# Optimization experiments

Measured on AMD Instinct MI355X. Metric: run time of the kernel, lower is better.

Reference implementation:

```python
import jax, jax.numpy as jnp
import numpy as np

NUM_HEADS = 8

def setup_inputs() -> dict:
    key0 = jax.random.key(0)
    ks = jax.random.split(key0, 6)
    T, S, B, E = 2048, 2048, 2, 256
    W_SCALE = 0.06  # ~xavier_uniform std for 256x256
    return {
        "query": jax.random.normal(ks[0], (T, B, E), dtype=jnp.float32),
        "key": jax.random.normal(ks[1], (S, B, E), dtype=jnp.float32),
        "value": jax.random.normal(ks[2], (S, B, E), dtype=jnp.float32),
        "Wq": jax.random.normal(ks[3], (E, E), dtype=jnp.float32) * W_SCALE,
        "bq": jnp.zeros((E,), dtype=jnp.float32),
        "Wk": jax.random.normal(ks[4], (E, E), dtype=jnp.float32) * W_SCALE,
        "bk": jnp.zeros((E,), dtype=jnp.float32),
        "Wo": jax.random.normal(ks[5], (E, E), dtype=jnp.float32) * W_SCALE,
        "bo": jnp.zeros((E,), dtype=jnp.float32),
    }

def reference(query, key, value, Wq, bq, Wk, bk, Wo, bo):
    # query: [T,B,E], key/value: [S,B,E]
    T, B, E = query.shape
    S = key.shape[0]
    H = NUM_HEADS
    Dh = E // H
    q = jnp.einsum('tbe,fe->tbf', query, Wq) + bq
    k = jnp.einsum('sbe,fe->sbf', key, Wk) + bk
    # split heads: view(L, B*H, Dh) == reshape(L, B, H, Dh)
    qh = q.reshape(T, B, H, Dh)
    kh = k.reshape(S, B, H, Dh)
    vh = value.reshape(S, B, H, Dh)  # v is NOT projected in this module
    scale = 1.0 / jnp.sqrt(jnp.asarray(Dh, dtype=query.dtype))
    scores = jnp.einsum('tbhd,sbhd->bhts', qh * scale, kh)  # [B,H,T,S]
    attn = jax.nn.softmax(scores, axis=-1)
    out = jnp.einsum('bhts,sbhd->tbhd', attn, vh).reshape(T, B, E)
    # residual output projection: out + linear(out)
    out = out + jnp.einsum('tbe,fe->tbf', out, Wo) + bo
    avg_weights = jnp.mean(attn, axis=1)  # [B,T,S]
    return (out, avg_weights)
```

## Files before the change

### kernel.cpp

```cpp
#include <hip/hip_runtime.h>
#include <hip/hip_fp16.h>

#define T_DIM 2048
#define S_DIM 2048
#define B_DIM 2
#define E_DIM 256
#define H_DIM 8
#define DH 32

typedef _Float16 half8 __attribute__((ext_vector_type(8)));
typedef _Float16 half4 __attribute__((ext_vector_type(4)));
typedef float floatx4 __attribute__((ext_vector_type(4)));

#if defined(__has_builtin)
#if __has_builtin(__builtin_amdgcn_exp2f)
#define EXPFN(x) __builtin_amdgcn_exp2f(x)
#define LOG2E_FOLD 1.4426950408889634f
#endif
#endif
#ifndef EXPFN
#define EXPFN(x) __expf(x)
#define LOG2E_FOLD 1.0f
#endif

__global__ __launch_bounds__(256) void prep_kernel(const float* __restrict__ V,
                                                   _Float16* __restrict__ Vt2,
                                                   const float* __restrict__ Wq,
                                                   const float* __restrict__ Wk,
                                                   const float* __restrict__ Wo,
                                                   _Float16* __restrict__ Wqh,
                                                   _Float16* __restrict__ Wkh,
                                                   _Float16* __restrict__ Woh) {
  __shared__ float tile[64][33];
  int tid = threadIdx.x;
  int bx = blockIdx.x;
  if (bx < 512) {
    int st = bx & 31, h = (bx >> 5) & 7, b = bx >> 8;
    int s0 = st * 64;
    int d = tid & 31, sr = tid >> 5;
#pragma unroll
    for (int k = 0; k < 8; ++k) {
      int s = sr + k * 8;
      tile[s][d] = V[((size_t)(s0 + s) * B_DIM + b) * E_DIM + h * DH + d];
    }
    __syncthreads();
    int si = tid & 63, dq = tid >> 6;
    size_t base = ((size_t)b * H_DIM + h) * 128 * 512;
    int tl = st * 4 + (si >> 4);
    int sl = si & 15;
#pragma unroll
    for (int m = 0; m < 8; ++m) {
      int dd = dq * 8 + m;
      Vt2[base + (size_t)tl * 512 + dd * 16 + sl] = (_Float16)tile[si][dd];
    }
  } else {
    int i = (bx - 512) * 2048 + tid * 8;
    int sel = i >> 16, off = i & 65535;
    const float* src = sel == 0 ? Wq : (sel == 1 ? Wk : Wo);
    _Float16* dst = sel == 0 ? Wqh : (sel == 1 ? Wkh : Woh);
    float4 a0 = *(const float4*)(src + off);
    float4 a1 = *(const float4*)(src + off + 4);
    half8 hv;
    hv[0]=(_Float16)a0.x; hv[1]=(_Float16)a0.y; hv[2]=(_Float16)a0.z; hv[3]=(_Float16)a0.w;
    hv[4]=(_Float16)a1.x; hv[5]=(_Float16)a1.y; hv[6]=(_Float16)a1.z; hv[7]=(_Float16)a1.w;
    if (sel == 2) {
      int f = off >> 8, e0 = off & 255;
      int di = f - e0;
      if (di >= 0 && di < 8) hv[di] += (_Float16)1.0f;
    }
    *(half8*)(dst + off) = hv;
  }
}

#define XS 264
__global__ __launch_bounds__(256, 4) void proj_mfma(const float* __restrict__ Q,
                                                    const float* __restrict__ K,
                                                    const _Float16* __restrict__ Wqh,
                                                    const _Float16* __restrict__ Wkh,
                                                    const float* __restrict__ bq,
                                                    const float* __restrict__ bk,
                                                    _Float16* __restrict__ Qp,
                                                    _Float16* __restrict__ Kp,
                                                    float scale_q) {
  __shared__ _Float16 Xs[64 * XS];
  int z = blockIdx.z;
  const float* X = z ? K : Q;
  const _Float16* Wh = z ? Wkh : Wqh;
  const float* bias = z ? bk : bq;
  _Float16* out = z ? Kp : Qp;
  float scale = z ? 1.0f : scale_q;

  int tid = threadIdx.x;
  int lane = tid & 63, w = tid >> 6;
  int quad = lane >> 4, l16 = lane & 15;
  int r0 = blockIdx.x * 64;
  int c0 = blockIdx.y * 64;

#pragma unroll
  for (int it = 0; it < 16; ++it) {
    int row = (tid >> 6) + it * 4, col = (tid & 63) * 4;
    float4 a = *(const float4*)(X + (size_t)(r0 + row) * 256 + col);
    half4 hv;
    hv[0] = (_Float16)a.x; hv[1] = (_Float16)a.y;
    hv[2] = (_Float16)a.z; hv[3] = (_Float16)a.w;
    *(half4*)(Xs + row * XS + col) = hv;
  }
  __syncthreads();

  floatx4 c[4] = {{0.f,0.f,0.f,0.f},{0.f,0.f,0.f,0.f},{0.f,0.f,0.f,0.f},{0.f,0.f,0.f,0.f}};
  int arow = w * 16 + l16;
#pragma unroll
  for (int k0 = 0; k0 < 256; k0 += 32) {
    half8 af = *(const half8*)(Xs + arow * XS + k0 + quad * 8);
#pragma unroll
    for (int j = 0; j < 4; ++j) {
      int f = c0 + j * 16 + l16;
      half8 bf = *(const half8*)(Wh + (size_t)f * 256 + k0 + quad * 8);
      c[j] = __builtin_amdgcn_mfma_f32_16x16x32_f16(af, bf, c[j], 0, 0, 0);
    }
  }
#pragma unroll
  for (int j = 0; j < 4; ++j) {
    int f = c0 + j * 16 + l16;
    float bv = bias[f];
    int h = f >> 5, d = f & 31;
#pragma unroll
    for (int r = 0; r < 4; ++r) {
      int row = r0 + w * 16 + quad * 4 + r;
      int t = row >> 1, b = row & 1;
      out[(((size_t)b * H_DIM + h) * T_DIM + t) * DH + d] =
          (_Float16)((c[j][r] + bv) * scale);
    }
  }
}

#define OSTRIDE 36
__global__ __launch_bounds__(1024, 4) void attn_fused(const _Float16* __restrict__ Qp,
                                                      const _Float16* __restrict__ Kp,
                                                      const _Float16* __restrict__ Vt2,
                                                      _Float16* __restrict__ Of16,
                                                      float* __restrict__ avg_out) {
  __shared__ float stageO[2][16][16 * OSTRIDE];
  __shared__ float lstage[2][16][16];

  int tid = threadIdx.x;
  int lane = tid & 63, w = tid >> 6;
  int quad = lane >> 4, l16 = lane & 15;
  int bx = blockIdx.x;
  int b = bx & 1, tc = bx >> 1;
  int t0 = tc << 4;
  int sbase = w << 7;
  int tl0 = w << 3;

  half4 avg_acc[8];
#pragma unroll
  for (int st = 0; st < 8; ++st) avg_acc[st] = (half4){0, 0, 0, 0};

  for (int h = 0; h < H_DIM; ++h) {
    const _Float16* Qb = Qp + (((size_t)b * H_DIM + h) * T_DIM + t0) * DH;
    const _Float16* Kb = Kp + ((size_t)b * H_DIM + h) * S_DIM * DH;
    const _Float16* Vb = Vt2 + ((size_t)b * H_DIM + h) * 128 * 512;

    half8 qfrag = *(const half8*)(Qb + (size_t)l16 * DH + quad * 8);
    floatx4 o0 = {0.f,0.f,0.f,0.f}, o1 = {0.f,0.f,0.f,0.f};
    float lacc = 0.f;
    half4 pst[8];

    half8 kf[2];
    half4 v0[2], v1[2];
    kf[0] = *(const half8*)(Kb + (size_t)(sbase + l16) * DH + quad * 8);
    v0[0] = *(const half4*)(Vb + (size_t)tl0 * 512 + l16 * 16 + quad * 4);
    v1[0] = *(const half4*)(Vb + (size_t)tl0 * 512 + 256 + l16 * 16 + quad * 4);

#pragma unroll
    for (int st = 0; st < 8; ++st) {
      int cur = st & 1, nxt = cur ^ 1;
      if (st < 7) {
        int tl = tl0 + st + 1;
        kf[nxt] = *(const half8*)(Kb + (size_t)(tl * 16 + l16) * DH + quad * 8);
        v0[nxt] = *(const half4*)(Vb + (size_t)tl * 512 + l16 * 16 + quad * 4);
        v1[nxt] = *(const half4*)(Vb + (size_t)tl * 512 + 256 + l16 * 16 + quad * 4);
      }
      floatx4 c = {0.f, 0.f, 0.f, 0.f};
      c = __builtin_amdgcn_mfma_f32_16x16x32_f16(kf[cur], qfrag, c, 0, 0, 0);
      float e0 = EXPFN(c[0]), e1 = EXPFN(c[1]), e2 = EXPFN(c[2]), e3 = EXPFN(c[3]);
      lacc += (e0 + e1) + (e2 + e3);
      half4 p;
      p[0] = (_Float16)e0; p[1] = (_Float16)e1; p[2] = (_Float16)e2; p[3] = (_Float16)e3;
      pst[st] = p;
      o0 = __builtin_amdgcn_mfma_f32_16x16x16f16(p, v0[cur], o0, 0, 0, 0);
      o1 = __builtin_amdgcn_mfma_f32_16x16x16f16(p, v1[cur], o1, 0, 0, 0);
    }

    int bufi = h & 1;
    lacc += __shfl_xor(lacc, 16, 64);
    lacc += __shfl_xor(lacc, 32, 64);
    if (quad == 0) lstage[bufi][w][l16] = lacc;
#pragma unroll
    for (int r = 0; r < 4; ++r) {
      stageO[bufi][w][(quad * 4 + r) * OSTRIDE + l16] = o0[r];
      stageO[bufi][w][(quad * 4 + r) * OSTRIDE + 16 + l16] = o1[r];
    }
    __syncthreads();

    float lrow = 0.f;
#pragma unroll
    for (int ww = 0; ww < 16; ++ww) lrow += lstage[bufi][ww][l16];
    _Float16 rlh = (_Float16)(1.0f / lrow);
    half4 rv; rv[0] = rlh; rv[1] = rlh; rv[2] = rlh; rv[3] = rlh;
#pragma unroll
    for (int st = 0; st < 8; ++st) avg_acc[st] += pst[st] * rv;

    if (tid < 512) {
      int t = tid >> 5, d = tid & 31;
      float osum = 0.f, lr = 0.f;
#pragma unroll
      for (int ww = 0; ww < 16; ++ww) {
        osum += stageO[bufi][ww][t * OSTRIDE + d];
        lr += lstage[bufi][ww][t];
      }
      Of16[((size_t)(t0 + t) * B_DIM + b) * E_DIM + h * DH + d] =
          (_Float16)(osum / lr);
    }
  }

  float* ao = avg_out + ((size_t)b * T_DIM + t0 + l16) * S_DIM + sbase + quad * 4;
#pragma unroll
  for (int st = 0; st < 8; ++st) {
    float4 o;
    o.x = (float)avg_acc[st][0] * 0.125f;
    o.y = (float)avg_acc[st][1] * 0.125f;
    o.z = (float)avg_acc[st][2] * 0.125f;
    o.w = (float)avg_acc[st][3] * 0.125f;
    *(float4*)(ao + st * 16) = o;
  }
}

__global__ __launch_bounds__(256, 4) void outproj_mfma(const _Float16* __restrict__ Of16,
                                                       const _Float16* __restrict__ Woh,
                                                       const float* __restrict__ bo,
                                                       float* __restrict__ out) {
  __shared__ _Float16 Os[64 * XS];
  int tid = threadIdx.x;
  int lane = tid & 63, w = tid >> 6;
  int quad = lane >> 4, l16 = lane & 15;
  int r0 = blockIdx.x * 64;
  int c0 = blockIdx.y * 64;

#pragma unroll
  for (int it = 0; it < 8; ++it) {
    int row = (tid >> 5) + it * 8, col = (tid & 31) * 8;
    *(half8*)(Os + row * XS + col) =
        *(const half8*)(Of16 + (size_t)(r0 + row) * 256 + col);
  }
  __syncthreads();

  floatx4 c[4] = {{0.f,0.f,0.f,0.f},{0.f,0.f,0.f,0.f},{0.f,0.f,0.f,0.f},{0.f,0.f,0.f,0.f}};
  int arow = w * 16 + l16;
#pragma unroll
  for (int k0 = 0; k0 < 256; k0 += 32) {
    half8 af = *(const half8*)(Os + arow * XS + k0 + quad * 8);
#pragma unroll
    for (int j = 0; j < 4; ++j) {
      int f = c0 + j * 16 + l16;
      half8 bf = *(const half8*)(Woh + (size_t)f * 256 + k0 + quad * 8);
      c[j] = __builtin_amdgcn_mfma_f32_16x16x32_f16(af, bf, c[j], 0, 0, 0);
    }
  }
#pragma unroll
  for (int j = 0; j < 4; ++j) {
    int f = c0 + j * 16 + l16;
    float bv = bo[f];
#pragma unroll
    for (int r = 0; r < 4; ++r) {
      int row = r0 + w * 16 + quad * 4 + r;
      out[(size_t)row * 256 + f] = c[j][r] + bv;
    }
  }
}

extern "C" void kernel_launch(void* const* d_in, const int* in_sizes, int n_in,
                              void* d_out, int out_size, void* d_ws, size_t ws_size,
                              hipStream_t stream) {
  const float* query = (const float*)d_in[0];
  const float* key   = (const float*)d_in[1];
  const float* value = (const float*)d_in[2];
  const float* Wq    = (const float*)d_in[3];
  const float* bq    = (const float*)d_in[4];
  const float* Wk    = (const float*)d_in[5];
  const float* bk    = (const float*)d_in[6];
  const float* Wo    = (const float*)d_in[7];
  const float* bo    = (const float*)d_in[8];

  float* out = (float*)d_out;
  float* avg_out = out + (size_t)T_DIM * B_DIM * E_DIM;

  char* ws = (char*)d_ws;
  _Float16* Qp   = (_Float16*)ws;
  _Float16* Kp   = (_Float16*)(ws + (2u << 20));
  _Float16* Vt2  = (_Float16*)(ws + (4u << 20));
  _Float16* Of16 = (_Float16*)(ws + (6u << 20));
  _Float16* Wqh  = (_Float16*)(ws + (8u << 20) + (128u << 10));
  _Float16* Wkh  = (_Float16*)(ws + (8u << 20) + (256u << 10));
  _Float16* Woh  = (_Float16*)(ws + (8u << 20) + (384u << 10));

  const float scale_q = 0.17677669529663687f * LOG2E_FOLD;

  prep_kernel<<<dim3(608), dim3(256), 0, stream>>>(value, Vt2, Wq, Wk, Wo, Wqh, Wkh, Woh);
  proj_mfma<<<dim3(64, 4, 2), dim3(256), 0, stream>>>(query, key, Wqh, Wkh, bq, bk,
                                                      Qp, Kp, scale_q);
  attn_fused<<<dim3(256), dim3(1024), 0, stream>>>(Qp, Kp, Vt2, Of16, avg_out);
  outproj_mfma<<<dim3(64, 4), dim3(256), 0, stream>>>(Of16, Woh, bo, out);
}
```

Before: 146.7 us.

## Fuse prep with QK projection and fold output projection into attention kernel

Measured after the change: 149.4 us. No clear change (+1.8%).

```diff
diff --git a/kernel.cpp b/kernel.cpp
--- a/kernel.cpp
+++ b/kernel.cpp
@@ -23,18 +23,24 @@
 #define LOG2E_FOLD 1.0f
 #endif
 
-__global__ __launch_bounds__(256) void prep_kernel(const float* __restrict__ V,
-                                                   _Float16* __restrict__ Vt2,
-                                                   const float* __restrict__ Wq,
-                                                   const float* __restrict__ Wk,
-                                                   const float* __restrict__ Wo,
-                                                   _Float16* __restrict__ Wqh,
-                                                   _Float16* __restrict__ Wkh,
-                                                   _Float16* __restrict__ Woh) {
-  __shared__ float tile[64][33];
+#define XS 264
+__global__ __launch_bounds__(256, 4) void prep_proj(const float* __restrict__ V,
+                                                    _Float16* __restrict__ Vt2,
+                                                    const float* __restrict__ Wo,
+                                                    _Float16* __restrict__ Woh,
+                                                    const float* __restrict__ Q,
+                                                    const float* __restrict__ K,
+                                                    const float* __restrict__ Wq,
+                                                    const float* __restrict__ Wk,
+                                                    const float* __restrict__ bq,
+                                                    const float* __restrict__ bk,
+                                                    _Float16* __restrict__ Qp,
+                                                    _Float16* __restrict__ Kp,
+                                                    float scale_q) {
   int tid = threadIdx.x;
   int bx = blockIdx.x;
   if (bx < 512) {
+    __shared__ float tile[64][33];
     int st = bx & 31, h = (bx >> 5) & 7, b = bx >> 8;
     int s0 = st * 64;
     int d = tid & 31, sr = tid >> 5;
@@ -53,83 +59,75 @@
       int dd = dq * 8 + m;
       Vt2[base + (size_t)tl * 512 + dd * 16 + sl] = (_Float16)tile[si][dd];
     }
-  } else {
+  } else if (bx < 544) {
     int i = (bx - 512) * 2048 + tid * 8;
-    int sel = i >> 16, off = i & 65535;
-    const float* src = sel == 0 ? Wq : (sel == 1 ? Wk : Wo);
-    _Float16* dst = sel == 0 ? Wqh : (sel == 1 ? Wkh : Woh);
-    float4 a0 = *(const float4*)(src + off);
-    float4 a1 = *(const float4*)(src + off + 4);
+    float4 a0 = *(const float4*)(Wo + i);
+    float4 a1 = *(const float4*)(Wo + i + 4);
     half8 hv;
     hv[0]=(_Float16)a0.x; hv[1]=(_Float16)a0.y; hv[2]=(_Float16)a0.z; hv[3]=(_Float16)a0.w;
     hv[4]=(_Float16)a1.x; hv[5]=(_Float16)a1.y; hv[6]=(_Float16)a1.z; hv[7]=(_Float16)a1.w;
-    if (sel == 2) {
-      int f = off >> 8, e0 = off & 255;
-      int di = f - e0;
-      if (di >= 0 && di < 8) hv[di] += (_Float16)1.0f;
-    }
-    *(half8*)(dst + off) = hv;
-  }
-}
-
-#define XS 264
-__global__ __launch_bounds__(256, 4) void proj_mfma(const float* __restrict__ Q,
-                                                    const float* __restrict__ K,
-                                                    const _Float16* __restrict__ Wqh,
-                                                    const _Float16* __restrict__ Wkh,
-                                                    const float* __restrict__ bq,
-                                                    const float* __restrict__ bk,
-                                                    _Float16* __restrict__ Qp,
-                                                    _Float16* __restrict__ Kp,
-                                                    float scale_q) {
-  __shared__ _Float16 Xs[64 * XS];
-  int z = blockIdx.z;
-  const float* X = z ? K : Q;
-  const _Float16* Wh = z ? Wkh : Wqh;
-  const float* bias = z ? bk : bq;
-  _Float16* out = z ? Kp : Qp;
-  float scale = z ? 1.0f : scale_q;
-
-  int tid = threadIdx.x;
-  int lane = tid & 63, w = tid >> 6;
-  int quad = lane >> 4, l16 = lane & 15;
-  int r0 = blockIdx.x * 64;
-  int c0 = blockIdx.y * 64;
-
-#pragma unroll
-  for (int it = 0; it < 16; ++it) {
-    int row = (tid >> 6) + it * 4, col = (tid & 63) * 4;
-    float4 a = *(const float4*)(X + (size_t)(r0 + row) * 256 + col);
-    half4 hv;
-    hv[0] = (_Float16)a.x; hv[1] = (_Float16)a.y;
-    hv[2] = (_Float16)a.z; hv[3] = (_Float16)a.w;
-    *(half4*)(Xs + row * XS + col) = hv;
-  }
-  __syncthreads();
-
-  floatx4 c[4] = {{0.f,0.f,0.f,0.f},{0.f,0.f,0.f,0.f},{0.f,0.f,0.f,0.f},{0.f,0.f,0.f,0.f}};
-  int arow = w * 16 + l16;
-#pragma unroll
-  for (int k0 = 0; k0 < 256; k0 += 32) {
-    half8 af = *(const half8*)(Xs + arow * XS + k0 + quad * 8);
-#pragma unroll
-    for (int j = 0; j < 4; ++j) {
+    int f = i >> 8, e0 = i & 255;
+    int di = f - e0;
+    if (di >= 0 && di < 8) hv[di] += (_Float16)1.0f;
+    *(half8*)(Woh + i) = hv;
+  } else {
+    __shared__ _Float16 Xs[64 * XS];
+    int idx = bx - 544;
+    int z = idx >> 7;
+    int rr = idx & 127;
+    int r0 = (rr >> 1) * 64;
+    int c0 = (rr & 1) * 128;
+    const float* X = z ? K : Q;
+    const float* W = z ? Wk : Wq;
+    const float* bias = z ? bk : bq;
+    _Float16* outp = z ? Kp : Qp;
+    float scale = z ? 1.0f : scale_q;
+
+    int lane = tid & 63, w = tid >> 6;
+    int quad = lane >> 4, l16 = lane & 15;
+
+#pragma unroll
+    for (int it = 0; it < 16; ++it) {
+      int row = (tid >> 6) + it * 4, col = (tid & 63) * 4;
+      float4 a = *(const float4*)(X + (size_t)(r0 + row) * 256 + col);
+      half4 hv;
+      hv[0] = (_Float16)a.x; hv[1] = (_Float16)a.y;
+      hv[2] = (_Float16)a.z; hv[3] = (_Float16)a.w;
+      *(half4*)(Xs + row * XS + col) = hv;
+    }
+    __syncthreads();
+
+    floatx4 c[8];
+#pragma unroll
+    for (int j = 0; j < 8; ++j) c[j] = (floatx4){0.f, 0.f, 0.f, 0.f};
+    int arow = w * 16 + l16;
+#pragma unroll
+    for (int k0 = 0; k0 < 256; k0 += 32) {
+      half8 af = *(const half8*)(Xs + arow * XS + k0 + quad * 8);
+#pragma unroll
+      for (int j = 0; j < 8; ++j) {
+        int f = c0 + j * 16 + l16;
+        const float* bp = W + (size_t)f * 256 + k0 + quad * 8;
+        float4 b0 = *(const float4*)bp;
+        float4 b1 = *(const float4*)(bp + 4);
+        half8 bf;
+        bf[0]=(_Float16)b0.x; bf[1]=(_Float16)b0.y; bf[2]=(_Float16)b0.z; bf[3]=(_Float16)b0.w;
+        bf[4]=(_Float16)b1.x; bf[5]=(_Float16)b1.y; bf[6]=(_Float16)b1.z; bf[7]=(_Float16)b1.w;
+        c[j] = __builtin_amdgcn_mfma_f32_16x16x32_f16(af, bf, c[j], 0, 0, 0);
+      }
+    }
+#pragma unroll
+    for (int j = 0; j < 8; ++j) {
       int f = c0 + j * 16 + l16;
-      half8 bf = *(const half8*)(Wh + (size_t)f * 256 + k0 + quad * 8);
-      c[j] = __builtin_amdgcn_mfma_f32_16x16x32_f16(af, bf, c[j], 0, 0, 0);
-    }
-  }
-#pragma unroll
-  for (int j = 0; j < 4; ++j) {
-    int f = c0 + j * 16 + l16;
-    float bv = bias[f];
-    int h = f >> 5, d = f & 31;
-#pragma unroll
-    for (int r = 0; r < 4; ++r) {
-      int row = r0 + w * 16 + quad * 4 + r;
-      int t = row >> 1, b = row & 1;
-      out[(((size_t)b * H_DIM + h) * T_DIM + t) * DH + d] =
-          (_Float16)((c[j][r] + bv) * scale);
+      float bv = bias[f];
+      int h = f >> 5, d = f & 31;
+#pragma unroll
+      for (int r = 0; r < 4; ++r) {
+        int row = r0 + w * 16 + quad * 4 + r;
+        int t = row >> 1, b = row & 1;
+        outp[(((size_t)b * H_DIM + h) * T_DIM + t) * DH + d] =
+            (_Float16)((c[j][r] + bv) * scale);
+      }
     }
   }
 }
@@ -138,10 +136,13 @@
 __global__ __launch_bounds__(1024, 4) void attn_fused(const _Float16* __restrict__ Qp,
                                                       const _Float16* __restrict__ Kp,
                                                       const _Float16* __restrict__ Vt2,
-                                                      _Float16* __restrict__ Of16,
+                                                      const _Float16* __restrict__ Woh,
+                                                      const float* __restrict__ bo,
+                                                      float* __restrict__ out,
                                                       float* __restrict__ avg_out) {
   __shared__ float stageO[2][16][16 * OSTRIDE];
   __shared__ float lstage[2][16][16];
+  __shared__ _Float16 Ost[16 * XS];
 
   int tid = threadIdx.x;
   int lane = tid & 63, w = tid >> 6;
@@ -152,45 +153,60 @@
   int sbase = w << 7;
   int tl0 = w << 3;
 
+  const size_t QH = (size_t)T_DIM * DH, KH = (size_t)S_DIM * DH, VH = 128 * 512;
+  const _Float16* Qb = Qp + ((size_t)b * H_DIM) * QH + (size_t)(t0 + l16) * DH + quad * 8;
+  const _Float16* Kb = Kp + ((size_t)b * H_DIM) * KH + (size_t)l16 * DH + quad * 8;
+  const _Float16* Vb = Vt2 + ((size_t)b * H_DIM) * VH + l16 * 16 + quad * 4;
+
   half4 avg_acc[8];
 #pragma unroll
   for (int st = 0; st < 8; ++st) avg_acc[st] = (half4){0, 0, 0, 0};
 
+  half8 qr = *(const half8*)Qb;
+  half8 qrn = qr;
+  half8 kf[4];
+  half4 v0[4], v1[4];
+#pragma unroll
+  for (int i = 0; i < 4; ++i) {
+    kf[i] = *(const half8*)(Kb + (size_t)(tl0 + i) * 16 * DH);
+    v0[i] = *(const half4*)(Vb + (size_t)(tl0 + i) * 512);
+    v1[i] = *(const half4*)(Vb + (size_t)(tl0 + i) * 512 + 256);
+  }
+
   for (int h = 0; h < H_DIM; ++h) {
-    const _Float16* Qb = Qp + (((size_t)b * H_DIM + h) * T_DIM + t0) * DH;
-    const _Float16* Kb = Kp + ((size_t)b * H_DIM + h) * S_DIM * DH;
-    const _Float16* Vb = Vt2 + ((size_t)b * H_DIM + h) * 128 * 512;
-
-    half8 qfrag = *(const half8*)(Qb + (size_t)l16 * DH + quad * 8);
     floatx4 o0 = {0.f,0.f,0.f,0.f}, o1 = {0.f,0.f,0.f,0.f};
     float lacc = 0.f;
     half4 pst[8];
 
-    half8 kf[2];
-    half4 v0[2], v1[2];
-    kf[0] = *(const half8*)(Kb + (size_t)(sbase + l16) * DH + quad * 8);
-    v0[0] = *(const half4*)(Vb + (size_t)tl0 * 512 + l16 * 16 + quad * 4);
-    v1[0] = *(const half4*)(Vb + (size_t)tl0 * 512 + 256 + l16 * 16 + quad * 4);
-
 #pragma unroll
     for (int st = 0; st < 8; ++st) {
-      int cur = st & 1, nxt = cur ^ 1;
-      if (st < 7) {
-        int tl = tl0 + st + 1;
-        kf[nxt] = *(const half8*)(Kb + (size_t)(tl * 16 + l16) * DH + quad * 8);
-        v0[nxt] = *(const half4*)(Vb + (size_t)tl * 512 + l16 * 16 + quad * 4);
-        v1[nxt] = *(const half4*)(Vb + (size_t)tl * 512 + 256 + l16 * 16 + quad * 4);
+      int slot = st & 3;
+      half8 kc = kf[slot];
+      half4 vc0 = v0[slot], vc1 = v1[slot];
+      if (st < 4) {
+        int tl = tl0 + st + 4;
+        kf[slot] = *(const half8*)(Kb + (size_t)tl * 16 * DH);
+        v0[slot] = *(const half4*)(Vb + (size_t)tl * 512);
+        v1[slot] = *(const half4*)(Vb + (size_t)tl * 512 + 256);
+      } else if (h + 1 < H_DIM) {
+        int tl = tl0 + st - 4;
+        kf[slot] = *(const half8*)(Kb + KH + (size_t)tl * 16 * DH);
+        v0[slot] = *(const half4*)(Vb + VH + (size_t)tl * 512);
+        v1[slot] = *(const half4*)(Vb + VH + (size_t)tl * 512 + 256);
+        if (st == 4) qrn = *(const half8*)(Qb + QH);
       }
       floatx4 c = {0.f, 0.f, 0.f, 0.f};
-      c = __builtin_amdgcn_mfma_f32_16x16x32_f16(kf[cur], qfrag, c, 0, 0, 0);
+      c = __builtin_amdgcn_mfma_f32_16x16x32_f16(kc, qr, c, 0, 0, 0);
       float e0 = EXPFN(c[0]), e1 = EXPFN(c[1]), e2 = EXPFN(c[2]), e3 = EXPFN(c[3]);
       lacc += (e0 + e1) + (e2 + e3);
       half4 p;
       p[0] = (_Float16)e0; p[1] = (_Float16)e1; p[2] = (_Float16)e2; p[3] = (_Float16)e3;
       pst[st] = p;
-      o0 = __builtin_amdgcn_mfma_f32_16x16x16f16(p, v0[cur], o0, 0, 0, 0);
-      o1 = __builtin_amdgcn_mfma_f32_16x16x16f16(p, v1[cur], o1, 0, 0, 0);
-    }
+      o0 = __builtin_amdgcn_mfma_f32_16x16x16f16(p, vc0, o0, 0, 0, 0);
+      o1 = __builtin_amdgcn_mfma_f32_16x16x16f16(p, vc1, o1, 0, 0, 0);
+    }
+    qr = qrn;
+    Qb += QH; Kb += KH; Vb += VH;
 
     int bufi = h & 1;
     lacc += __shfl_xor(lacc, 16, 64);
@@ -219,8 +235,25 @@
         osum += stageO[bufi][ww][t * OSTRIDE + d];
         lr += lstage[bufi][ww][t];
       }
-      Of16[((size_t)(t0 + t) * B_DIM + b) * E_DIM + h * DH + d] =
-          (_Float16)(osum / lr);
+      Ost[t * XS + h * DH + d] = (_Float16)(osum / lr);
+    }
+  }
+  __syncthreads();
+
+  {
+    floatx4 oc = {0.f, 0.f, 0.f, 0.f};
+    int f = w * 16 + l16;
+#pragma unroll
+    for (int k0 = 0; k0 < 256; k0 += 32) {
+      half8 af = *(const half8*)(Ost + l16 * XS + k0 + quad * 8);
+      half8 bf = *(const half8*)(Woh + (size_t)f * 256 + k0 + quad * 8);
+      oc = __builtin_amdgcn_mfma_f32_16x16x32_f16(af, bf, oc, 0, 0, 0);
+    }
+    float bv = bo[f];
+#pragma unroll
+    for (int r = 0; r < 4; ++r) {
+      int t = quad * 4 + r;
+      out[((size_t)(t0 + t) * B_DIM + b) * E_DIM + f] = oc[r] + bv;
     }
   }
 
@@ -233,49 +266,6 @@
     o.z = (float)avg_acc[st][2] * 0.125f;
     o.w = (float)avg_acc[st][3] * 0.125f;
     *(float4*)(ao + st * 16) = o;
-  }
-}
-
-__global__ __launch_bounds__(256, 4) void outproj_mfma(const _Float16* __restrict__ Of16,
-                                                       const _Float16* __restrict__ Woh,
-                                                       const float* __restrict__ bo,
-                                                       float* __restrict__ out) {
-  __shared__ _Float16 Os[64 * XS];
-  int tid = threadIdx.x;
-  int lane = tid & 63, w = tid >> 6;
-  int quad = lane >> 4, l16 = lane & 15;
-  int r0 = blockIdx.x * 64;
-  int c0 = blockIdx.y * 64;
-
-#pragma unroll
-  for (int it = 0; it < 8; ++it) {
-    int row = (tid >> 5) + it * 8, col = (tid & 31) * 8;
-    *(half8*)(Os + row * XS + col) =
-        *(const half8*)(Of16 + (size_t)(r0 + row) * 256 + col);
-  }
-  __syncthreads();
-
-  floatx4 c[4] = {{0.f,0.f,0.f,0.f},{0.f,0.f,0.f,0.f},{0.f,0.f,0.f,0.f},{0.f,0.f,0.f,0.f}};
-  int arow = w * 16 + l16;
-#pragma unroll
-  for (int k0 = 0; k0 < 256; k0 += 32) {
-    half8 af = *(const half8*)(Os + arow * XS + k0 + quad * 8);
-#pragma unroll
-    for (int j = 0; j < 4; ++j) {
-      int f = c0 + j * 16 + l16;
-      half8 bf = *(const half8*)(Woh + (size_t)f * 256 + k0 + quad * 8);
-      c[j] = __builtin_amdgcn_mfma_f32_16x16x32_f16(af, bf, c[j], 0, 0, 0);
-    }
-  }
-#pragma unroll
-  for (int j = 0; j < 4; ++j) {
-    int f = c0 + j * 16 + l16;
-    float bv = bo[f];
-#pragma unroll
-    for (int r = 0; r < 4; ++r) {
-      int row = r0 + w * 16 + quad * 4 + r;
-      out[(size_t)row * 256 + f] = c[j][r] + bv;
-    }
   }
 }
 
@@ -296,19 +286,16 @@
   float* avg_out = out + (size_t)T_DIM * B_DIM * E_DIM;
 
   char* ws = (char*)d_ws;
-  _Float16* Qp   = (_Float16*)ws;
-  _Float16* Kp   = (_Float16*)(ws + (2u << 20));
-  _Float16* Vt2  = (_Float16*)(ws + (4u << 20));
-  _Float16* Of16 = (_Float16*)(ws + (6u << 20));
-  _Float16* Wqh  = (_Float16*)(ws + (8u << 20) + (128u << 10));
-  _Float16* Wkh  = (_Float16*)(ws + (8u << 20) + (256u << 10));
-  _Float16* Woh  = (_Float16*)(ws + (8u << 20) + (384u << 10));
+  _Float16* Qp  = (_Float16*)ws;
+  _Float16* Kp  = (_Float16*)(ws + (2u << 20));
+  _Float16* Vt2 = (_Float16*)(ws + (4u << 20));
+  _Float16* Woh = (_Float16*)(ws + (6u << 20));
 
   const float scale_q = 0.17677669529663687f * LOG2E_FOLD;
 
-  prep_kernel<<<dim3(608), dim3(256), 0, stream>>>(value, Vt2, Wq, Wk, Wo, Wqh, Wkh, Woh);
-  proj_mfma<<<dim3(64, 4, 2), dim3(256), 0, stream>>>(query, key, Wqh, Wkh, bq, bk,
-                                                      Qp, Kp, scale_q);
-  attn_fused<<<dim3(256), dim3(1024), 0, stream>>>(Qp, Kp, Vt2, Of16, avg_out);
-  outproj_mfma<<<dim3(64, 4), dim3(256), 0, stream>>>(Of16, Woh, bo, out);
+  prep_proj<<<dim3(800), dim3(256), 0, stream>>>(value, Vt2, Wo, Woh,
+                                                 query, key, Wq, Wk, bq, bk,
+                                                 Qp, Kp, scale_q);
+  attn_fused<<<dim3(256), dim3(1024), 0, stream>>>(Qp, Kp, Vt2, Woh, bo,
+                                                   out, avg_out);
 }
```
